# Performance work log

Measured on AMD Instinct MI355X. Metric: run time of the kernel, lower is better.

The kernel has to match this reference:

```python
import jax, jax.numpy as jnp
import numpy as np

B, S, D, U = 4, 2048, 1024, 1024

def setup_inputs() -> dict:
    key = jax.random.key(0)
    k0, k1, k2, k3 = jax.random.split(key, 4)
    scale = 1.0 / np.sqrt(D)  # keep logits sane; Glorot-like magnitude
    return {
        "inputs": jax.random.normal(k0, (B, S, D), dtype=jnp.float32),
        "W_q": jax.random.normal(k1, (D, U), dtype=jnp.float32) * scale,
        "W_k": jax.random.normal(k2, (D, U), dtype=jnp.float32) * scale,
        "W_v": jax.random.normal(k3, (D, U), dtype=jnp.float32) * scale,
    }

def reference(inputs, W_q, W_k, W_v):
    # QKV projections: [B,S,D] @ [D,U] -> [B,S,U]
    q = jnp.einsum("bsd,du->bsu", inputs, W_q)
    k = jnp.einsum("bsd,du->bsu", inputs, W_k)
    v = jnp.einsum("bsd,du->bsu", inputs, W_v)
    # Unscaled attention, as in the source (no 1/sqrt(d) factor)
    scores = jnp.einsum("bqu,bku->bqk", q, k)          # [B,S,S]
    weights = jax.nn.softmax(scores, axis=-1)
    return jnp.einsum("bqk,bku->bqu", weights, v)       # [B,S,U]
```

## Files before the change

kernel.cpp:

```cpp
#include <hip/hip_runtime.h>
#include <cstdint>
#include <cstddef>


typedef unsigned short ushort_t;
typedef _Float16 half_t;
typedef __attribute__((ext_vector_type(8))) short short8;
typedef __attribute__((ext_vector_type(4))) float floatx4;

__device__ inline unsigned short h2u(half_t h) {
  union { half_t h; unsigned short u; } v; v.h = h; return v.u;
}

__device__ __forceinline__ void gload16(const half_t* g, half_t* l) {
  __builtin_amdgcn_global_load_lds(
      (const __attribute__((address_space(1))) unsigned int*)g,
      (__attribute__((address_space(3))) unsigned int*)l, 16, 0, 0);
}

#define BAR() asm volatile("s_barrier" ::: "memory")
#define LGKM0() asm volatile("s_waitcnt lgkmcnt(0)" ::: "memory")
#define VM8() asm volatile("s_waitcnt vmcnt(8)" ::: "memory")
#define VM4() asm volatile("s_waitcnt vmcnt(4)" ::: "memory")
#define VM0() asm volatile("s_waitcnt vmcnt(0)" ::: "memory")

#define MX 8192
#define KCAT 2048

#define XCAT_OFF 0UL
#define WT_OFF   50331648UL
#define S_OFF    0UL
#define QCAT_OFF 69206016UL
#define KCAT_OFF 119537664UL
#define VT_OFF   169869312UL
#define WS_NEED  186646528UL

#define XCD_REMAP(BX, BY, BZ)                                              \
  const int fbid_ = blockIdx.x + 8 * (blockIdx.y + gridDim.y * blockIdx.z); \
  const int xj_ = fbid_ & 7, xi_ = fbid_ >> 3;                              \
  const int BX = ((xj_ & 1) << 2) | (xi_ & 3);                              \
  const int nrow_ = (xj_ >> 1) * ((gridDim.y * gridDim.z) >> 2) + (xi_ >> 2);\
  const int BY = nrow_ % gridDim.y;                                         \
  const int BZ = nrow_ / gridDim.y;

__global__ __launch_bounds__(256) void k_split_x(const float* __restrict__ X,
                                                 half_t* __restrict__ xcat) {
  long long i = (long long)blockIdx.x * 256 + threadIdx.x;
  float x = X[i];
  half_t h = (half_t)x;
  half_t lo = (half_t)(x - (float)h);
  long long row = i >> 10;
  int col = (int)(i & 1023);
  half_t* r = xcat + row * KCAT;
  r[col] = h;
  r[col + 1024] = lo;
}

__global__ __launch_bounds__(256) void k_split_wt(const float* __restrict__ Wq,
                                                  const float* __restrict__ Wk,
                                                  const float* __restrict__ Wv,
                                                  half_t* __restrict__ wt) {
  __shared__ float tile[64][65];
  const float* W = (blockIdx.z == 0) ? Wq : ((blockIdx.z == 1) ? Wk : Wv);
  half_t* out = wt + (size_t)blockIdx.z * 1024 * KCAT;
  int d0 = blockIdx.y * 64, u0 = blockIdx.x * 64;
  int t = threadIdx.x;
  int tr = t >> 6, tc = t & 63;
  for (int r = 0; r < 64; r += 4)
    tile[r + tr][tc] = W[(size_t)(d0 + r + tr) * 1024 + (u0 + tc)];
  __syncthreads();
  for (int r = 0; r < 64; r += 4) {
    int urow = r + tr, dcol = tc;
    float x = tile[dcol][urow];
    half_t h = (half_t)x;
    half_t* o = out + (size_t)(u0 + urow) * KCAT + d0;
    o[dcol] = h;
    o[dcol + 1024] = h;
  }
}

enum { EP_F32 = 0, EP_QK = 1, EP_VT = 2 };

template <int MODE>
__global__ __launch_bounds__(256, 4) void k_gemm(
    const half_t* __restrict__ A, long long aBatch, int lda,
    const half_t* __restrict__ Bt, long long bBatch, int ldb,
    void* __restrict__ Cout, long long cBatch, int ldc, int K,
    half_t* __restrict__ CoutK) {
  __shared__ __align__(16) half_t As[128 * 64];
  __shared__ __align__(16) half_t Bs[128 * 64];
  const int t = threadIdx.x;
  XCD_REMAP(bx, by, z);
  A += (long long)z * aBatch;
  Bt += (long long)z * bBatch;
  const int m0 = by * 128, n0 = bx * 128;

  const int w = t >> 6, l = t & 63;
  const int lr = l & 15, quad = l >> 4;
  const int wm = (w >> 1) * 64, wn = (w & 1) * 64;

  const floatx4 fz = {0.f, 0.f, 0.f, 0.f};
  floatx4 acc[4][4];
#pragma unroll
  for (int i = 0; i < 4; i++)
#pragma unroll
    for (int j = 0; j < 4; j++) acc[i][j] = fz;

  const half_t* Ap[4];
  const half_t* Bp[4];
  half_t* ldsA[4];
  half_t* ldsB[4];
#pragma unroll
  for (int s = 0; s < 4; s++) {
    int c = s * 256 + t;
    int row = c >> 3, gq = (c & 7) ^ ((c >> 3) & 7);
    Ap[s] = A + (long long)(m0 + row) * lda + gq * 8;
    Bp[s] = Bt + (long long)(n0 + row) * ldb + gq * 8;
    ldsA[s] = &As[(s * 256 + w * 64) * 8];
    ldsB[s] = &Bs[(s * 256 + w * 64) * 8];
  }

  const int p0 = quad ^ (lr & 7);
  const int p1 = (quad + 4) ^ (lr & 7);
  const int arow = (wm + lr) * 64, brow = (wn + lr) * 64;

  for (int kb = 0; kb < K; kb += 64) {
    __syncthreads();
#pragma unroll
    for (int s = 0; s < 4; s++) {
      gload16(Ap[s] + kb, ldsA[s]);
      gload16(Bp[s] + kb, ldsB[s]);
    }
    __syncthreads();
#pragma unroll
    for (int s = 0; s < 2; s++) {
      const int pp = s ? p1 : p0;
      short8 af[4], bfg[4];
#pragma unroll
      for (int j = 0; j < 4; j++) bfg[j] = *(const short8*)&Bs[brow + j * 1024 + pp * 8];
#pragma unroll
      for (int i = 0; i < 4; i++) af[i] = *(const short8*)&As[arow + i * 1024 + pp * 8];
#pragma unroll
      for (int i = 0; i < 4; i++)
#pragma unroll
        for (int j = 0; j < 4; j++)
          acc[i][j] = __builtin_amdgcn_mfma_f32_16x16x32_f16(af[i], bfg[j], acc[i][j], 0, 0, 0);
    }
  }

#pragma unroll
  for (int i = 0; i < 4; i++) {
#pragma unroll
    for (int j = 0; j < 4; j++) {
#pragma unroll
      for (int r = 0; r < 4; r++) {
        int grow = m0 + wm + i * 16 + quad * 4 + r;
        int gcol = n0 + wn + j * 16 + lr;
        float v = acc[i][j][r];
        if (MODE == EP_F32) {
          float* C = (float*)Cout + (long long)z * cBatch;
          C[(long long)grow * ldc + gcol] = v;
        } else {
          half_t* C = (half_t*)Cout;
          int b = grow >> 11, s = grow & 2047;
          C[((long long)b * 1024 + gcol) * 2048 + s] = (half_t)v;
        }
      }
    }
  }
}

template <int MODE>
__global__ __launch_bounds__(512, 2) void k_gemm256(
    const half_t* __restrict__ A, long long aBatch, int lda,
    const half_t* __restrict__ Bt, long long bBatch, int ldb,
    void* __restrict__ Cout, long long cBatch, int ldc, int K,
    half_t* __restrict__ CoutK) {
  __shared__ __align__(16) half_t As[32768];
  __shared__ __align__(16) half_t Bs[32768];
  const int tid = threadIdx.x;
  XCD_REMAP(bx, by, z);
  A += (long long)z * aBatch;
  Bt += (long long)z * bBatch;
  const int m0 = by * 256, n0 = bx * 256;
  const int w = tid >> 6, l = tid & 63;
  const int lr = l & 15, quad = l >> 4;
  const int wm = w >> 2, wn = w & 3;

  const floatx4 fz = {0.f, 0.f, 0.f, 0.f};
  floatx4 acc[8][4];
#pragma unroll
  for (int i = 0; i < 8; i++)
#pragma unroll
    for (int j = 0; j < 4; j++) acc[i][j] = fz;

  const int r0 = tid >> 2;
  const int gq0 = (tid & 3) ^ ((tid >> 3) & 3);
  const half_t* aS0 = A + (long long)(m0 + r0) * lda + gq0 * 8;
  const half_t* aS1 = aS0 + (long long)128 * lda;
  const half_t* bS0 = Bt + (long long)(n0 + r0) * ldb + gq0 * 8;
  const half_t* bS1 = bS0 + (long long)128 * ldb;
  const int wso = w << 9;

  const int swz = (quad ^ ((lr >> 1) & 3)) << 3;
  const int aBase = wm * 4096 + lr * 32 + swz;
  const int bBase = wn * 2048 + lr * 32 + swz;
  const int NT = K >> 6;

#define SA(BUF, KH, KOFF) do { half_t* d_ = &As[(BUF) * 16384 + (KH) * 8192 + wso]; \
    gload16(aS0 + (KOFF), d_); gload16(aS1 + (KOFF), d_ + 4096); } while (0)
#define SB(BUF, KH, KOFF) do { half_t* d_ = &Bs[(BUF) * 16384 + (KH) * 8192 + wso]; \
    gload16(bS0 + (KOFF), d_); gload16(bS1 + (KOFF), d_ + 4096); } while (0)
#define LDA4(S, OFF) { const half_t* ap_ = &As[(OFF)]; \
    S##0 = *(const short8*)(ap_); S##1 = *(const short8*)(ap_ + 512); \
    S##2 = *(const short8*)(ap_ + 1024); S##3 = *(const short8*)(ap_ + 1536); }
#define LDB4(S, OFF) { const half_t* bp_ = &Bs[(OFF)]; \
    S##0 = *(const short8*)(bp_); S##1 = *(const short8*)(bp_ + 512); \
    S##2 = *(const short8*)(bp_ + 1024); S##3 = *(const short8*)(bp_ + 1536); }
#define MFMA16(I0, AS, BS) do { \
    acc[(I0) + 0][0] = __builtin_amdgcn_mfma_f32_16x16x32_f16(AS##0, BS##0, acc[(I0) + 0][0], 0, 0, 0); \
    acc[(I0) + 0][1] = __builtin_amdgcn_mfma_f32_16x16x32_f16(AS##0, BS##1, acc[(I0) + 0][1], 0, 0, 0); \
    acc[(I0) + 0][2] = __builtin_amdgcn_mfma_f32_16x16x32_f16(AS##0, BS##2, acc[(I0) + 0][2], 0, 0, 0); \
    acc[(I0) + 0][3] = __builtin_amdgcn_mfma_f32_16x16x32_f16(AS##0, BS##3, acc[(I0) + 0][3], 0, 0, 0); \
    acc[(I0) + 1][0] = __builtin_amdgcn_mfma_f32_16x16x32_f16(AS##1, BS##0, acc[(I0) + 1][0], 0, 0, 0); \
    acc[(I0) + 1][1] = __builtin_amdgcn_mfma_f32_16x16x32_f16(AS##1, BS##1, acc[(I0) + 1][1], 0, 0, 0); \
    acc[(I0) + 1][2] = __builtin_amdgcn_mfma_f32_16x16x32_f16(AS##1, BS##2, acc[(I0) + 1][2], 0, 0, 0); \
    acc[(I0) + 1][3] = __builtin_amdgcn_mfma_f32_16x16x32_f16(AS##1, BS##3, acc[(I0) + 1][3], 0, 0, 0); \
    acc[(I0) + 2][0] = __builtin_amdgcn_mfma_f32_16x16x32_f16(AS##2, BS##0, acc[(I0) + 2][0], 0, 0, 0); \
    acc[(I0) + 2][1] = __builtin_amdgcn_mfma_f32_16x16x32_f16(AS##2, BS##1, acc[(I0) + 2][1], 0, 0, 0); \
    acc[(I0) + 2][2] = __builtin_amdgcn_mfma_f32_16x16x32_f16(AS##2, BS##2, acc[(I0) + 2][2], 0, 0, 0); \
    acc[(I0) + 2][3] = __builtin_amdgcn_mfma_f32_16x16x32_f16(AS##2, BS##3, acc[(I0) + 2][3], 0, 0, 0); \
    acc[(I0) + 3][0] = __builtin_amdgcn_mfma_f32_16x16x32_f16(AS##3, BS##0, acc[(I0) + 3][0], 0, 0, 0); \
    acc[(I0) + 3][1] = __builtin_amdgcn_mfma_f32_16x16x32_f16(AS##3, BS##1, acc[(I0) + 3][1], 0, 0, 0); \
    acc[(I0) + 3][2] = __builtin_amdgcn_mfma_f32_16x16x32_f16(AS##3, BS##2, acc[(I0) + 3][2], 0, 0, 0); \
    acc[(I0) + 3][3] = __builtin_amdgcn_mfma_f32_16x16x32_f16(AS##3, BS##3, acc[(I0) + 3][3], 0, 0, 0); \
  } while (0)

  SB(0, 0, 0); SA(0, 0, 0); SB(0, 1, 32); SA(0, 1, 32);
  SA(1, 0, 64); SB(1, 0, 64);
  VM8();
  BAR();

  for (int t = 0; t < NT; ++t) {
    const int buf = t & 1, nbuf = buf ^ 1;
    const int ab = buf * 16384;
    const int kb = t * 64;

    {
      short8 aA0, aA1, aA2, aA3, aB0, aB1, aB2, aB3, bA0, bA1, bA2, bA3;
      LDA4(aA, ab + aBase);
      LDA4(aB, ab + aBase + 2048);
      LDB4(bA, ab + bBase);
      if (t + 1 < NT) {
        SA(nbuf, 1, kb + 96);
        SB(nbuf, 1, kb + 96);
        VM8();
      } else {
        VM0();
      }
      BAR(); LGKM0();
      __builtin_amdgcn_s_setprio(1);
      MFMA16(0, aA, bA);
      MFMA16(4, aB, bA);
      __builtin_amdgcn_s_setprio(0);
      BAR();
    }

    {
      short8 aA0, aA1, aA2, aA3, aB0, aB1, aB2, aB3, bA0, bA1, bA2, bA3;
      LDA4(aA, ab + 8192 + aBase);
      LDA4(aB, ab + 8192 + aBase + 2048);
      LDB4(bA, ab + 8192 + bBase);
      if (t + 2 < NT) {
        SA(buf, 0, kb + 128);
        SB(buf, 0, kb + 128);
        VM8();
      } else if (t + 1 < NT) {
        VM4();
      }
      BAR(); LGKM0();
      __builtin_amdgcn_s_setprio(1);
      MFMA16(0, aA, bA);
      MFMA16(4, aB, bA);
      __builtin_amdgcn_s_setprio(0);
      BAR();
    }
  }

#pragma unroll
  for (int i = 0; i < 8; i++) {
#pragma unroll
    for (int j = 0; j < 4; j++) {
#pragma unroll
      for (int r = 0; r < 4; r++) {
        int grow = m0 + wm * 128 + i * 16 + quad * 4 + r;
        int gcol = n0 + wn * 64 + j * 16 + lr;
        float v = acc[i][j][r];
        if (MODE == EP_F32) {
          float* C = (float*)Cout + (long long)z * cBatch;
          C[(long long)grow * ldc + gcol] = v;
        } else {
          int sel = gcol >> 10;
          int ucol = gcol & 1023;
          half_t h = (half_t)v;
          unsigned hu = h2u(h);
          unsigned val;
          half_t* base;
          if (sel == 0) {
            val = hu | ((unsigned)h2u((half_t)(v - (float)h)) << 16);
            base = (half_t*)Cout;
          } else {
            val = hu | (hu << 16);
            base = CoutK;
          }
          *(unsigned*)(base + (long long)grow * KCAT + 2 * ucol) = val;
        }
      }
    }
  }
#undef SA
#undef SB
#undef LDA4
#undef LDB4
#undef MFMA16
}

__global__ __launch_bounds__(256) void k_softmax(float* __restrict__ Sbuf) {
  long long row = blockIdx.x;
  float* p = Sbuf + row * 2048;
  int t = threadIdx.x;
  float4 v0 = ((const float4*)p)[t];
  float4 v1 = ((const float4*)p)[t + 256];
  float m = fmaxf(fmaxf(fmaxf(v0.x, v0.y), fmaxf(v0.z, v0.w)),
                  fmaxf(fmaxf(v1.x, v1.y), fmaxf(v1.z, v1.w)));
  for (int off = 32; off; off >>= 1) m = fmaxf(m, __shfl_xor(m, off));
  __shared__ float red[8];
  int wv = t >> 6, ln = t & 63;
  if (ln == 0) red[wv] = m;
  __syncthreads();
  m = fmaxf(fmaxf(red[0], red[1]), fmaxf(red[2], red[3]));
  float e0 = __expf(v0.x - m), e1 = __expf(v0.y - m), e2 = __expf(v0.z - m), e3 = __expf(v0.w - m);
  float e4 = __expf(v1.x - m), e5 = __expf(v1.y - m), e6 = __expf(v1.z - m), e7 = __expf(v1.w - m);
  float s = ((e0 + e1) + (e2 + e3)) + ((e4 + e5) + (e6 + e7));
  for (int off = 32; off; off >>= 1) s += __shfl_xor(s, off);
  if (ln == 0) red[4 + wv] = s;
  __syncthreads();
  s = (red[4] + red[5]) + (red[6] + red[7]);
  float inv = 1.0f / s;
  uint2 w0, w1;
  w0.x = (unsigned)h2u((half_t)(e0 * inv)) | ((unsigned)h2u((half_t)(e1 * inv)) << 16);
  w0.y = (unsigned)h2u((half_t)(e2 * inv)) | ((unsigned)h2u((half_t)(e3 * inv)) << 16);
  w1.x = (unsigned)h2u((half_t)(e4 * inv)) | ((unsigned)h2u((half_t)(e5 * inv)) << 16);
  w1.y = (unsigned)h2u((half_t)(e6 * inv)) | ((unsigned)h2u((half_t)(e7 * inv)) << 16);
  ((uint2*)p)[t] = w0;
  ((uint2*)p)[t + 256] = w1;
}

extern "C" void kernel_launch(void* const* d_in, const int* in_sizes, int n_in,
                              void* d_out, int out_size, void* d_ws, size_t ws_size,
                              hipStream_t stream) {
  (void)in_sizes; (void)n_in; (void)out_size;
  if (ws_size < WS_NEED) return;

  const float* X = (const float*)d_in[0];
  const float* Wq = (const float*)d_in[1];
  const float* Wk = (const float*)d_in[2];
  const float* Wv = (const float*)d_in[3];
  char* ws = (char*)d_ws;
  half_t* xcat = (half_t*)(ws + XCAT_OFF);
  half_t* wt = (half_t*)(ws + WT_OFF);
  float* Sbuf = (float*)(ws + S_OFF);
  half_t* qcat = (half_t*)(ws + QCAT_OFF);
  half_t* kcat = (half_t*)(ws + KCAT_OFF);
  half_t* vt = (half_t*)(ws + VT_OFF);
  float* out = (float*)d_out;

  k_split_x<<<dim3(MX * 1024 / 256), dim3(256), 0, stream>>>(X, xcat);
  k_split_wt<<<dim3(16, 16, 3), dim3(256), 0, stream>>>(Wq, Wk, Wv, wt);

  k_gemm256<EP_QK><<<dim3(8, 32, 1), dim3(512), 0, stream>>>(
      xcat, 0LL, KCAT, wt, 0LL, KCAT, qcat, 0LL, 0, KCAT, kcat);

  k_gemm<EP_VT><<<dim3(8, 64, 1), dim3(256), 0, stream>>>(
      xcat, 0LL, KCAT, wt + 2 * 1024 * KCAT, 0LL, KCAT, vt, 0LL, 0, 1024, nullptr);

  k_gemm256<EP_F32><<<dim3(8, 8, 4), dim3(512), 0, stream>>>(
      qcat, (long long)2048 * KCAT, KCAT, kcat, (long long)2048 * KCAT, KCAT,
      Sbuf, (long long)2048 * 2048, 2048, KCAT, nullptr);

  k_softmax<<<dim3(8192), dim3(256), 0, stream>>>(Sbuf);

  k_gemm<EP_F32><<<dim3(8, 16, 4), dim3(256), 0, stream>>>(
      (const half_t*)Sbuf, (long long)2048 * 4096, 4096,
      vt, (long long)1024 * 2048, 2048,
      out, (long long)2048 * 1024, 1024, 2048, nullptr);
}
```

Baseline: 315.0 us.

## Shrink gemm256 tile to 256x128 with 3-stage K=32 pipeline

Changes the big GEMM kernel from a 256x256 tile with a 64-deep K double buffer to a 256x128 tile with a 3-buffer ring of K=32 slices. Launch bounds are raised to four blocks per CU, the grids are doubled in x, and a new XCD remap is added for 16-wide grids. The aim is more resident blocks and finer-grained load/compute overlap with a single barrier per step. In exchange, each block gets less operand reuse and global traffic per FLOP goes up.

New measurement: 313.9 us. About the same (-0.3%).

```diff
diff --git a/kernel.cpp b/kernel.cpp
--- a/kernel.cpp
+++ b/kernel.cpp
@@ -20,8 +20,7 @@
 
 #define BAR() asm volatile("s_barrier" ::: "memory")
 #define LGKM0() asm volatile("s_waitcnt lgkmcnt(0)" ::: "memory")
-#define VM8() asm volatile("s_waitcnt vmcnt(8)" ::: "memory")
-#define VM4() asm volatile("s_waitcnt vmcnt(4)" ::: "memory")
+#define VM3() asm volatile("s_waitcnt vmcnt(3)" ::: "memory")
 #define VM0() asm volatile("s_waitcnt vmcnt(0)" ::: "memory")
 
 #define MX 8192
@@ -42,6 +41,14 @@
   const int nrow_ = (xj_ >> 1) * ((gridDim.y * gridDim.z) >> 2) + (xi_ >> 2);\
   const int BY = nrow_ % gridDim.y;                                         \
   const int BZ = nrow_ / gridDim.y;
+
+#define XCD_REMAP16(BX, BY, BZ)                                             \
+  const int fb_ = blockIdx.x + 16 * (blockIdx.y + gridDim.y * blockIdx.z);  \
+  const int xj_ = fb_ & 7, xi_ = fb_ >> 3;                                  \
+  const int BX = (xj_ & 3) * 4 + (xi_ & 3);                                 \
+  const int nr_ = (xj_ >> 2) * 16 + (xi_ >> 2);                             \
+  const int BY = nr_ % gridDim.y;                                           \
+  const int BZ = nr_ / gridDim.y;
 
 __global__ __launch_bounds__(256) void k_split_x(const float* __restrict__ X,
                                                  half_t* __restrict__ xcat) {
@@ -171,26 +178,26 @@
 }
 
 template <int MODE>
-__global__ __launch_bounds__(512, 2) void k_gemm256(
+__global__ __launch_bounds__(512, 4) void k_gemm256(
     const half_t* __restrict__ A, long long aBatch, int lda,
     const half_t* __restrict__ Bt, long long bBatch, int ldb,
     void* __restrict__ Cout, long long cBatch, int ldc, int K,
     half_t* __restrict__ CoutK) {
-  __shared__ __align__(16) half_t As[32768];
-  __shared__ __align__(16) half_t Bs[32768];
+  __shared__ __align__(16) half_t As[24576];
+  __shared__ __align__(16) half_t Bs[12288];
   const int tid = threadIdx.x;
-  XCD_REMAP(bx, by, z);
+  XCD_REMAP16(bx, by, z);
   A += (long long)z * aBatch;
   Bt += (long long)z * bBatch;
-  const int m0 = by * 256, n0 = bx * 256;
+  const int m0 = by * 256, n0 = bx * 128;
   const int w = tid >> 6, l = tid & 63;
   const int lr = l & 15, quad = l >> 4;
-  const int wm = w >> 2, wn = w & 3;
+  const int wm = w >> 1, wn = w & 1;
 
   const floatx4 fz = {0.f, 0.f, 0.f, 0.f};
-  floatx4 acc[8][4];
-#pragma unroll
-  for (int i = 0; i < 8; i++)
+  floatx4 acc[4][4];
+#pragma unroll
+  for (int i = 0; i < 4; i++)
 #pragma unroll
     for (int j = 0; j < 4; j++) acc[i][j] = fz;
 
@@ -199,101 +206,75 @@
   const half_t* aS0 = A + (long long)(m0 + r0) * lda + gq0 * 8;
   const half_t* aS1 = aS0 + (long long)128 * lda;
   const half_t* bS0 = Bt + (long long)(n0 + r0) * ldb + gq0 * 8;
-  const half_t* bS1 = bS0 + (long long)128 * ldb;
   const int wso = w << 9;
 
   const int swz = (quad ^ ((lr >> 1) & 3)) << 3;
-  const int aBase = wm * 4096 + lr * 32 + swz;
+  const int aBase = wm * 2048 + lr * 32 + swz;
   const int bBase = wn * 2048 + lr * 32 + swz;
-  const int NT = K >> 6;
-
-#define SA(BUF, KH, KOFF) do { half_t* d_ = &As[(BUF) * 16384 + (KH) * 8192 + wso]; \
+  const int NT = K >> 5;
+
+#define SA(BUF, KOFF) do { half_t* d_ = &As[(BUF) * 8192 + wso]; \
     gload16(aS0 + (KOFF), d_); gload16(aS1 + (KOFF), d_ + 4096); } while (0)
-#define SB(BUF, KH, KOFF) do { half_t* d_ = &Bs[(BUF) * 16384 + (KH) * 8192 + wso]; \
-    gload16(bS0 + (KOFF), d_); gload16(bS1 + (KOFF), d_ + 4096); } while (0)
+#define SB(BUF, KOFF) do { half_t* d_ = &Bs[(BUF) * 4096 + wso]; \
+    gload16(bS0 + (KOFF), d_); } while (0)
 #define LDA4(S, OFF) { const half_t* ap_ = &As[(OFF)]; \
     S##0 = *(const short8*)(ap_); S##1 = *(const short8*)(ap_ + 512); \
     S##2 = *(const short8*)(ap_ + 1024); S##3 = *(const short8*)(ap_ + 1536); }
 #define LDB4(S, OFF) { const half_t* bp_ = &Bs[(OFF)]; \
     S##0 = *(const short8*)(bp_); S##1 = *(const short8*)(bp_ + 512); \
     S##2 = *(const short8*)(bp_ + 1024); S##3 = *(const short8*)(bp_ + 1536); }
-#define MFMA16(I0, AS, BS) do { \
-    acc[(I0) + 0][0] = __builtin_amdgcn_mfma_f32_16x16x32_f16(AS##0, BS##0, acc[(I0) + 0][0], 0, 0, 0); \
-    acc[(I0) + 0][1] = __builtin_amdgcn_mfma_f32_16x16x32_f16(AS##0, BS##1, acc[(I0) + 0][1], 0, 0, 0); \
-    acc[(I0) + 0][2] = __builtin_amdgcn_mfma_f32_16x16x32_f16(AS##0, BS##2, acc[(I0) + 0][2], 0, 0, 0); \
-    acc[(I0) + 0][3] = __builtin_amdgcn_mfma_f32_16x16x32_f16(AS##0, BS##3, acc[(I0) + 0][3], 0, 0, 0); \
-    acc[(I0) + 1][0] = __builtin_amdgcn_mfma_f32_16x16x32_f16(AS##1, BS##0, acc[(I0) + 1][0], 0, 0, 0); \
-    acc[(I0) + 1][1] = __builtin_amdgcn_mfma_f32_16x16x32_f16(AS##1, BS##1, acc[(I0) + 1][1], 0, 0, 0); \
-    acc[(I0) + 1][2] = __builtin_amdgcn_mfma_f32_16x16x32_f16(AS##1, BS##2, acc[(I0) + 1][2], 0, 0, 0); \
-    acc[(I0) + 1][3] = __builtin_amdgcn_mfma_f32_16x16x32_f16(AS##1, BS##3, acc[(I0) + 1][3], 0, 0, 0); \
-    acc[(I0) + 2][0] = __builtin_amdgcn_mfma_f32_16x16x32_f16(AS##2, BS##0, acc[(I0) + 2][0], 0, 0, 0); \
-    acc[(I0) + 2][1] = __builtin_amdgcn_mfma_f32_16x16x32_f16(AS##2, BS##1, acc[(I0) + 2][1], 0, 0, 0); \
-    acc[(I0) + 2][2] = __builtin_amdgcn_mfma_f32_16x16x32_f16(AS##2, BS##2, acc[(I0) + 2][2], 0, 0, 0); \
-    acc[(I0) + 2][3] = __builtin_amdgcn_mfma_f32_16x16x32_f16(AS##2, BS##3, acc[(I0) + 2][3], 0, 0, 0); \
-    acc[(I0) + 3][0] = __builtin_amdgcn_mfma_f32_16x16x32_f16(AS##3, BS##0, acc[(I0) + 3][0], 0, 0, 0); \
-    acc[(I0) + 3][1] = __builtin_amdgcn_mfma_f32_16x16x32_f16(AS##3, BS##1, acc[(I0) + 3][1], 0, 0, 0); \
-    acc[(I0) + 3][2] = __builtin_amdgcn_mfma_f32_16x16x32_f16(AS##3, BS##2, acc[(I0) + 3][2], 0, 0, 0); \
-    acc[(I0) + 3][3] = __builtin_amdgcn_mfma_f32_16x16x32_f16(AS##3, BS##3, acc[(I0) + 3][3], 0, 0, 0); \
+#define MFMA16(AS, BS) do { \
+    acc[0][0] = __builtin_amdgcn_mfma_f32_16x16x32_f16(AS##0, BS##0, acc[0][0], 0, 0, 0); \
+    acc[0][1] = __builtin_amdgcn_mfma_f32_16x16x32_f16(AS##0, BS##1, acc[0][1], 0, 0, 0); \
+    acc[0][2] = __builtin_amdgcn_mfma_f32_16x16x32_f16(AS##0, BS##2, acc[0][2], 0, 0, 0); \
+    acc[0][3] = __builtin_amdgcn_mfma_f32_16x16x32_f16(AS##0, BS##3, acc[0][3], 0, 0, 0); \
+    acc[1][0] = __builtin_amdgcn_mfma_f32_16x16x32_f16(AS##1, BS##0, acc[1][0], 0, 0, 0); \
+    acc[1][1] = __builtin_amdgcn_mfma_f32_16x16x32_f16(AS##1, BS##1, acc[1][1], 0, 0, 0); \
+    acc[1][2] = __builtin_amdgcn_mfma_f32_16x16x32_f16(AS##1, BS##2, acc[1][2], 0, 0, 0); \
+    acc[1][3] = __builtin_amdgcn_mfma_f32_16x16x32_f16(AS##1, BS##3, acc[1][3], 0, 0, 0); \
+    acc[2][0] = __builtin_amdgcn_mfma_f32_16x16x32_f16(AS##2, BS##0, acc[2][0], 0, 0, 0); \
+    acc[2][1] = __builtin_amdgcn_mfma_f32_16x16x32_f16(AS##2, BS##1, acc[2][1], 0, 0, 0); \
+    acc[2][2] = __builtin_amdgcn_mfma_f32_16x16x32_f16(AS##2, BS##2, acc[2][2], 0, 0, 0); \
+    acc[2][3] = __builtin_amdgcn_mfma_f32_16x16x32_f16(AS##2, BS##3, acc[2][3], 0, 0, 0); \
+    acc[3][0] = __builtin_amdgcn_mfma_f32_16x16x32_f16(AS##3, BS##0, acc[3][0], 0, 0, 0); \
+    acc[3][1] = __builtin_amdgcn_mfma_f32_16x16x32_f16(AS##3, BS##1, acc[3][1], 0, 0, 0); \
+    acc[3][2] = __builtin_amdgcn_mfma_f32_16x16x32_f16(AS##3, BS##2, acc[3][2], 0, 0, 0); \
+    acc[3][3] = __builtin_amdgcn_mfma_f32_16x16x32_f16(AS##3, BS##3, acc[3][3], 0, 0, 0); \
   } while (0)
 
-  SB(0, 0, 0); SA(0, 0, 0); SB(0, 1, 32); SA(0, 1, 32);
-  SA(1, 0, 64); SB(1, 0, 64);
-  VM8();
+  SA(0, 0); SB(0, 0);
+  SA(1, 32); SB(1, 32);
+  VM3();
   BAR();
 
+  int cur = 0;
   for (int t = 0; t < NT; ++t) {
-    const int buf = t & 1, nbuf = buf ^ 1;
-    const int ab = buf * 16384;
-    const int kb = t * 64;
-
-    {
-      short8 aA0, aA1, aA2, aA3, aB0, aB1, aB2, aB3, bA0, bA1, bA2, bA3;
-      LDA4(aA, ab + aBase);
-      LDA4(aB, ab + aBase + 2048);
-      LDB4(bA, ab + bBase);
-      if (t + 1 < NT) {
-        SA(nbuf, 1, kb + 96);
-        SB(nbuf, 1, kb + 96);
-        VM8();
-      } else {
-        VM0();
-      }
-      BAR(); LGKM0();
-      __builtin_amdgcn_s_setprio(1);
-      MFMA16(0, aA, bA);
-      MFMA16(4, aB, bA);
-      __builtin_amdgcn_s_setprio(0);
-      BAR();
-    }
-
-    {
-      short8 aA0, aA1, aA2, aA3, aB0, aB1, aB2, aB3, bA0, bA1, bA2, bA3;
-      LDA4(aA, ab + 8192 + aBase);
-      LDA4(aB, ab + 8192 + aBase + 2048);
-      LDB4(bA, ab + 8192 + bBase);
-      if (t + 2 < NT) {
-        SA(buf, 0, kb + 128);
-        SB(buf, 0, kb + 128);
-        VM8();
-      } else if (t + 1 < NT) {
-        VM4();
-      }
-      BAR(); LGKM0();
-      __builtin_amdgcn_s_setprio(1);
-      MFMA16(0, aA, bA);
-      MFMA16(4, aB, bA);
-      __builtin_amdgcn_s_setprio(0);
-      BAR();
-    }
-  }
-
-#pragma unroll
-  for (int i = 0; i < 8; i++) {
+    short8 aA0, aA1, aA2, aA3, bA0, bA1, bA2, bA3;
+    LDA4(aA, cur * 8192 + aBase);
+    LDB4(bA, cur * 4096 + bBase);
+    if (t + 2 < NT) {
+      const int sb = (cur >= 1) ? cur - 1 : 2;
+      SA(sb, (t + 2) * 32);
+      SB(sb, (t + 2) * 32);
+      VM3();
+    } else if (t == NT - 2) {
+      VM0();
+    }
+    BAR();
+    LGKM0();
+    __builtin_amdgcn_s_setprio(1);
+    MFMA16(aA, bA);
+    __builtin_amdgcn_s_setprio(0);
+    cur = (cur == 2) ? 0 : cur + 1;
+  }
+
+#pragma unroll
+  for (int i = 0; i < 4; i++) {
 #pragma unroll
     for (int j = 0; j < 4; j++) {
 #pragma unroll
       for (int r = 0; r < 4; r++) {
-        int grow = m0 + wm * 128 + i * 16 + quad * 4 + r;
+        int grow = m0 + wm * 64 + i * 16 + quad * 4 + r;
         int gcol = n0 + wn * 64 + j * 16 + lr;
         float v = acc[i][j][r];
         if (MODE == EP_F32) {
@@ -378,13 +359,13 @@
   k_split_x<<<dim3(MX * 1024 / 256), dim3(256), 0, stream>>>(X, xcat);
   k_split_wt<<<dim3(16, 16, 3), dim3(256), 0, stream>>>(Wq, Wk, Wv, wt);
 
-  k_gemm256<EP_QK><<<dim3(8, 32, 1), dim3(512), 0, stream>>>(
+  k_gemm256<EP_QK><<<dim3(16, 32, 1), dim3(512), 0, stream>>>(
       xcat, 0LL, KCAT, wt, 0LL, KCAT, qcat, 0LL, 0, KCAT, kcat);
 
   k_gemm<EP_VT><<<dim3(8, 64, 1), dim3(256), 0, stream>>>(
       xcat, 0LL, KCAT, wt + 2 * 1024 * KCAT, 0LL, KCAT, vt, 0LL, 0, 1024, nullptr);
 
-  k_gemm256<EP_F32><<<dim3(8, 8, 4), dim3(512), 0, stream>>>(
+  k_gemm256<EP_F32><<<dim3(16, 8, 4), dim3(512), 0, stream>>>(
       qcat, (long long)2048 * KCAT, KCAT, kcat, (long long)2048 * KCAT, KCAT,
       Sbuf, (long long)2048 * 2048, 2048, KCAT, nullptr);
 
```
